# Kernel tuning notes

Hardware: AMD Instinct MI355X
Metric: run time of the kernel (lower is better)

## Reference

```python
import jax, jax.numpy as jnp
import numpy as np
from jax import lax

B, P, ENC, DEC, ATT, EMB, V, L = 64, 196, 2048, 512, 512, 512, 10000, 30


def setup_inputs() -> dict:
    key = jax.random.key(0)
    ks = jax.random.split(key, 24)
    s = 0.02
    encoder_out = jax.random.normal(ks[0], (B, P, ENC), dtype=jnp.float32)
    encoded_captions = jax.random.randint(ks[1], (B, L), 0, V, dtype=jnp.int64)
    caption_lengths = jax.random.randint(ks[2], (B, 1), 2, L + 1, dtype=jnp.int64)
    # ensure max decode length == L-1 (matches torch max(decode_lengths))
    caption_lengths = caption_lengths.at[0, 0].set(L)
    p = lambda k, sh: jax.random.normal(k, sh, dtype=jnp.float32) * s
    return {
        "encoder_out": encoder_out,
        "encoded_captions": encoded_captions,
        "caption_lengths": caption_lengths,
        "W_enc": p(ks[3], (ATT, ENC)), "b_enc": jnp.zeros((ATT,), jnp.float32),
        "W_dec": p(ks[4], (ATT, DEC)), "b_dec": jnp.zeros((ATT,), jnp.float32),
        "w_full": p(ks[5], (ATT,)), "b_full": jnp.zeros((), jnp.float32),
        "emb_table": jax.random.uniform(ks[6], (V, EMB), jnp.float32, -0.1, 0.1),
        "W_ih": p(ks[7], (4 * DEC, EMB + ENC)), "b_ih": jnp.zeros((4 * DEC,), jnp.float32),
        "W_hh": p(ks[8], (4 * DEC, DEC)), "b_hh": jnp.zeros((4 * DEC,), jnp.float32),
        "W_init_h": p(ks[9], (DEC, ENC)), "b_init_h": jnp.zeros((DEC,), jnp.float32),
        "W_init_c": p(ks[10], (DEC, ENC)), "b_init_c": jnp.zeros((DEC,), jnp.float32),
        "W_beta": p(ks[11], (ENC, DEC)), "b_beta": jnp.zeros((ENC,), jnp.float32),
        "W_fc": jax.random.uniform(ks[12], (V, DEC), jnp.float32, -0.1, 0.1),
        "b_fc": jnp.zeros((V,), jnp.float32),
    }


def reference(encoder_out, encoded_captions, caption_lengths,
              W_enc, b_enc, W_dec, b_dec, w_full, b_full, emb_table,
              W_ih, b_ih, W_hh, b_hh, W_init_h, b_init_h, W_init_c, b_init_c,
              W_beta, b_beta, W_fc, b_fc):
    lengths = caption_lengths[:, 0]
    sort_ind = jnp.argsort(-lengths)  # descending, stable
    enc = encoder_out[sort_ind]            # [B,P,ENC]
    caps = encoded_captions[sort_ind]      # [B,L]
    dec_lens = lengths[sort_ind] - 1       # [B]
    T = caps.shape[1] - 1

    embs = emb_table[caps]                 # [B,L,EMB]
    mean_enc = enc.mean(axis=1)
    h0 = mean_enc @ W_init_h.T + b_init_h
    c0 = mean_enc @ W_init_c.T + b_init_c
    # encoder attention projection is h-independent: compute once
    att1 = jnp.einsum('bpe,ae->bpa', enc, W_enc) + b_enc  # [B,P,ATT]

    def step(carry, xs):
        h, c = carry
        emb_t, mask_t = xs  # [B,EMB], [B] bool
        att2 = h @ W_dec.T + b_dec                              # [B,ATT]
        e = jax.nn.relu(att1 + att2[:, None, :]) @ w_full + b_full  # [B,P]
        alpha = jax.nn.softmax(e, axis=1)
        awe = jnp.einsum('bp,bpe->be', alpha, enc)              # [B,ENC]
        gate = jax.nn.sigmoid(h @ W_beta.T + b_beta)
        awe = gate * awe
        x = jnp.concatenate([emb_t, awe], axis=1)               # [B,EMB+ENC]
        gates = x @ W_ih.T + b_ih + h @ W_hh.T + b_hh           # [B,4D]
        i, f, g, o = jnp.split(gates, 4, axis=1)
        i, f, o = jax.nn.sigmoid(i), jax.nn.sigmoid(f), jax.nn.sigmoid(o)
        g = jnp.tanh(g)
        c_new = f * c + i * g
        h_new = o * jnp.tanh(c_new)
        preds = h_new @ W_fc.T + b_fc                           # [B,V]  (dropout: eval/identity)
        m = mask_t[:, None].astype(preds.dtype)
        return (h_new, c_new), (preds * m, alpha * m)

    mask = jnp.arange(T)[:, None] < dec_lens[None, :]           # [T,B]
    embs_t = jnp.swapaxes(embs[:, :T], 0, 1)                    # [T,B,EMB]
    _, (preds, alphas) = lax.scan(step, (h0, c0), (embs_t, mask))
    predictions = jnp.swapaxes(preds, 0, 1)                     # [B,T,V]
    alphas = jnp.swapaxes(alphas, 0, 1)                         # [B,T,P]
    return predictions, alphas, caps, dec_lens, sort_ind
```

## Files before the change

### kernel.cpp

```cpp
#include <hip/hip_runtime.h>
#include <hip/hip_bf16.h>
#include <math.h>
#include <float.h>

#define BDIM   64
#define PDIM   196
#define ENC    2048
#define DECD   512
#define ATTD   512
#define EMBD   512
#define VOC    10000
#define LCAP   30
#define TSTEPS 29

typedef __attribute__((ext_vector_type(8))) short s8v;
typedef __attribute__((ext_vector_type(4))) float f4v;

__device__ __forceinline__ float sigf(float x) { return 1.0f / (1.0f + expf(-x)); }
__device__ __forceinline__ float bf2f(ushort u) { return __uint_as_float(((uint)u) << 16); }

template <int MF, int NIT>
__device__ __forceinline__ void gemm_seg(const __hip_bfloat16* const* arow,
                                         const __hip_bfloat16* const* wrow,
                                         f4v acc[][4]) {
    s8v aP[3][MF], bP[3][4];
    auto LD = [&](int it, int slot) {
#pragma unroll
        for (int mi = 0; mi < MF; ++mi) aP[slot][mi] = *(const s8v*)(arow[mi] + it * 32);
#pragma unroll
        for (int ni = 0; ni < 4; ++ni)  bP[slot][ni] = *(const s8v*)(wrow[ni] + it * 32);
    };
    LD(0, 0);
    if constexpr (NIT > 1) LD(1, 1);
#pragma unroll
    for (int it = 0; it < NIT; ++it) {
        if (it + 2 < NIT) LD(it + 2, (it + 2) % 3);
        const int s = it % 3;
#pragma unroll
        for (int mi = 0; mi < MF; ++mi)
#pragma unroll
            for (int ni = 0; ni < 4; ++ni)
                acc[mi][ni] = __builtin_amdgcn_mfma_f32_16x16x32_bf16(aP[s][mi], bP[s][ni], acc[mi][ni], 0, 0, 0);
    }
}

__global__ void sort_kernel(const int* __restrict__ cap_len,
                            const int* __restrict__ caps,
                            int* __restrict__ sort_ind,
                            int* __restrict__ dec_lens,
                            int* __restrict__ caps_s,
                            float* __restrict__ out_caps,
                            float* __restrict__ out_dlen,
                            float* __restrict__ out_sind) {
    int i = threadIdx.x;
    __shared__ int len[BDIM];
    len[i] = cap_len[i];
    __syncthreads();
    int li = len[i];
    int r = 0;
    for (int j = 0; j < BDIM; ++j) {
        int lj = len[j];
        if (lj > li || (lj == li && j < i)) ++r;
    }
    sort_ind[r] = i;
    dec_lens[r] = li - 1;
    out_sind[r] = (float)i;
    out_dlen[r] = (float)(li - 1);
    for (int tt = 0; tt < LCAP; ++tt) {
        int v = caps[i * LCAP + tt];
        caps_s[r * LCAP + tt] = v;
        out_caps[r * LCAP + tt] = (float)v;
    }
}

__global__ __launch_bounds__(256) void conv_enc_kernel(const float* __restrict__ enc,
                                                       const int* __restrict__ sort_ind,
                                                       __hip_bfloat16* __restrict__ enc_s,
                                                       float* __restrict__ mean_enc) {
    int b = blockIdx.y, tid = threadIdx.x;
    int e = (blockIdx.x << 8) + tid;
    const float* ep = enc + (size_t)sort_ind[b] * (PDIM * ENC) + e;
    __hip_bfloat16* op = enc_s + (size_t)b * (PDIM * ENC) + e;
    float s = 0.f;
    for (int p = 0; p < PDIM; ++p) {
        float v = ep[(size_t)p * ENC];
        s += v;
        op[(size_t)p * ENC] = __float2bfloat16(v);
    }
    mean_enc[(size_t)b * ENC + e] = s * (1.0f / (float)PDIM);
}

__global__ __launch_bounds__(256) void f2b_kernel(const float* __restrict__ src,
                                                  __hip_bfloat16* __restrict__ dst, int n) {
    int i = blockIdx.x * 256 + threadIdx.x;
    if (i < n) dst[i] = __float2bfloat16(src[i]);
}

__global__ __launch_bounds__(256) void h0_kernel(const float* __restrict__ h0f,
                                                 __hip_bfloat16* __restrict__ xh) {
    int idx = blockIdx.x * 256 + threadIdx.x;
    int b = idx >> 9, j = idx & 511;
    xh[(size_t)b * 3072 + 2560 + j] = __float2bfloat16(h0f[idx]);
}

__global__ __launch_bounds__(256) void gemm32_k(
    const float* __restrict__ A, int lda,
    const float* __restrict__ W0, const float* __restrict__ bias0,
    float* __restrict__ C, int ldc, int K) {
    __shared__ float As[16][64];
    __shared__ float Ws[16][64];
    const int tid = threadIdx.x;
    const int tx = tid & 15, ty = tid >> 4;
    const int bn0 = blockIdx.x * 64;
    const int lr = tid >> 2;
    const int lk = (tid & 3) << 2;
    const float* Arow = A + (size_t)lr * lda;
    const int wn = bn0 + lr;
    float acc[4][4];
#pragma unroll
    for (int i = 0; i < 4; ++i)
#pragma unroll
        for (int j = 0; j < 4; ++j) acc[i][j] = 0.f;
    for (int k0 = 0; k0 < K; k0 += 16) {
        float4 av = *(const float4*)(Arow + k0 + lk);
        float4 wv = *(const float4*)(W0 + (size_t)wn * K + k0 + lk);
        __syncthreads();
        As[lk + 0][lr] = av.x; As[lk + 1][lr] = av.y;
        As[lk + 2][lr] = av.z; As[lk + 3][lr] = av.w;
        Ws[lk + 0][lr] = wv.x; Ws[lk + 1][lr] = wv.y;
        Ws[lk + 2][lr] = wv.z; Ws[lk + 3][lr] = wv.w;
        __syncthreads();
#pragma unroll
        for (int kk = 0; kk < 16; ++kk) {
            const float4 a = *(const float4*)&As[kk][ty << 2];
            const float4 w = *(const float4*)&Ws[kk][tx << 2];
            acc[0][0] += a.x * w.x; acc[0][1] += a.x * w.y; acc[0][2] += a.x * w.z; acc[0][3] += a.x * w.w;
            acc[1][0] += a.y * w.x; acc[1][1] += a.y * w.y; acc[1][2] += a.y * w.z; acc[1][3] += a.y * w.w;
            acc[2][0] += a.z * w.x; acc[2][1] += a.z * w.y; acc[2][2] += a.z * w.z; acc[2][3] += a.z * w.w;
            acc[3][0] += a.w * w.x; acc[3][1] += a.w * w.y; acc[3][2] += a.w * w.z; acc[3][3] += a.w * w.w;
        }
    }
#pragma unroll
    for (int i = 0; i < 4; ++i) {
        int row = (ty << 2) + i;
#pragma unroll
        for (int j = 0; j < 4; ++j) {
            int col = bn0 + (tx << 2) + j;
            C[(size_t)row * ldc + col] = acc[i][j] + bias0[col];
        }
    }
}

__global__ __launch_bounds__(64) void att1_gemm(
    const __hip_bfloat16* __restrict__ A, const __hip_bfloat16* __restrict__ W,
    const float* __restrict__ bias, __hip_bfloat16* __restrict__ C) {
    const int l = threadIdx.x, c16 = l & 15, kg = l >> 4;
    const int m0 = blockIdx.x * 32, n0 = blockIdx.y * 64;
    f4v acc[2][4];
#pragma unroll
    for (int mi = 0; mi < 2; ++mi)
#pragma unroll
        for (int ni = 0; ni < 4; ++ni) acc[mi][ni] = (f4v)0.0f;
    const __hip_bfloat16* arow[2];
#pragma unroll
    for (int mi = 0; mi < 2; ++mi)
        arow[mi] = A + (size_t)(m0 + mi * 16 + c16) * ENC + kg * 8;
    const __hip_bfloat16* wrow[4];
#pragma unroll
    for (int ni = 0; ni < 4; ++ni)
        wrow[ni] = W + (size_t)(n0 + ni * 16 + c16) * ENC + kg * 8;
    gemm_seg<2, 64>(arow, wrow, acc);
#pragma unroll
    for (int mi = 0; mi < 2; ++mi)
#pragma unroll
        for (int ni = 0; ni < 4; ++ni)
#pragma unroll
            for (int i = 0; i < 4; ++i) {
                int r = m0 + mi * 16 + kg * 4 + i;
                int c = n0 + ni * 16 + c16;
                C[(size_t)r * 512 + c] = __float2bfloat16(acc[mi][ni][i] + bias[c]);
            }
}

__global__ __launch_bounds__(64) void gact_gemm(
    const __hip_bfloat16* __restrict__ H,
    const __hip_bfloat16* __restrict__ Wb,
    const __hip_bfloat16* __restrict__ Wd,
    float* __restrict__ P) {
    const int l = threadIdx.x, c16 = l & 15, kg = l >> 4;
    const int n0 = blockIdx.x * 64, m0 = blockIdx.y * 16, z = blockIdx.z;
    const int ko = z * 256;
    f4v acc[1][4];
#pragma unroll
    for (int ni = 0; ni < 4; ++ni) acc[0][ni] = (f4v)0.0f;
    const __hip_bfloat16* arow[1] = { H + (size_t)(m0 + c16) * 3072 + ko + kg * 8 };
    const __hip_bfloat16* wrow[4];
#pragma unroll
    for (int ni = 0; ni < 4; ++ni) {
        int n = n0 + ni * 16 + c16;
        wrow[ni] = ((n < 2048) ? Wb + (size_t)n * 512 : Wd + (size_t)(n - 2048) * 512) + ko + kg * 8;
    }
    gemm_seg<1, 8>(arow, wrow, acc);
    float* Pz = P + (size_t)z * (64 * 2560);
#pragma unroll
    for (int ni = 0; ni < 4; ++ni)
#pragma unroll
        for (int i = 0; i < 4; ++i) {
            int r = m0 + kg * 4 + i;
            int c = n0 + ni * 16 + c16;
            Pz[(size_t)r * 2560 + c] = acc[0][ni][i];
        }
}

__global__ __launch_bounds__(64) void gates_gemm(
    const __hip_bfloat16* __restrict__ X,
    const __hip_bfloat16* __restrict__ Wih,
    const __hip_bfloat16* __restrict__ Whh,
    float* __restrict__ P) {
    const int l = threadIdx.x, c16 = l & 15, kg = l >> 4;
    const int n0 = blockIdx.x * 64, m0 = blockIdx.y * 16, z = blockIdx.z;
    f4v acc[1][4];
#pragma unroll
    for (int ni = 0; ni < 4; ++ni) acc[0][ni] = (f4v)0.0f;
    const __hip_bfloat16* arow[1];
    const __hip_bfloat16* wrow[4];
    if (z == 0) {
        arow[0] = X + (size_t)(m0 + c16) * 3072 + kg * 8;
#pragma unroll
        for (int ni = 0; ni < 4; ++ni)
            wrow[ni] = Wih + (size_t)(n0 + ni * 16 + c16) * 2560 + kg * 8;
        gemm_seg<1, 48>(arow, wrow, acc);
    } else {
        arow[0] = X + (size_t)(m0 + c16) * 3072 + 1536 + kg * 8;
#pragma unroll
        for (int ni = 0; ni < 4; ++ni)
            wrow[ni] = Wih + (size_t)(n0 + ni * 16 + c16) * 2560 + 1536 + kg * 8;
        gemm_seg<1, 32>(arow, wrow, acc);
        arow[0] = X + (size_t)(m0 + c16) * 3072 + 2560 + kg * 8;
#pragma unroll
        for (int ni = 0; ni < 4; ++ni)
            wrow[ni] = Whh + (size_t)(n0 + ni * 16 + c16) * 512 + kg * 8;
        gemm_seg<1, 16>(arow, wrow, acc);
    }
    float* Pz = P + (size_t)z * (64 * 2048);
#pragma unroll
    for (int ni = 0; ni < 4; ++ni)
#pragma unroll
        for (int i = 0; i < 4; ++i) {
            int r = m0 + kg * 4 + i;
            int c = n0 + ni * 16 + c16;
            Pz[(size_t)r * 2048 + c] = acc[0][ni][i];
        }
}

__global__ __launch_bounds__(64) void predsb_gemm(
    const __hip_bfloat16* __restrict__ Hs,
    const __hip_bfloat16* __restrict__ Wfc,
    const float* __restrict__ bias,
    const int* __restrict__ dec_lens,
    float* __restrict__ out) {
    const int l = threadIdx.x, c16 = l & 15, kg = l >> 4;
    const int n0 = blockIdx.x * 64, m0 = blockIdx.y * 32;
    f4v acc[2][4];
#pragma unroll
    for (int mi = 0; mi < 2; ++mi)
#pragma unroll
        for (int ni = 0; ni < 4; ++ni) acc[mi][ni] = (f4v)0.0f;
    const __hip_bfloat16* arow[2];
#pragma unroll
    for (int mi = 0; mi < 2; ++mi)
        arow[mi] = Hs + (size_t)(m0 + mi * 16 + c16) * 512 + kg * 8;
    const __hip_bfloat16* wrow[4];
#pragma unroll
    for (int ni = 0; ni < 4; ++ni) {
        int n = n0 + ni * 16 + c16;
        int nn = (n < VOC) ? n : (VOC - 1);
        wrow[ni] = Wfc + (size_t)nn * 512 + kg * 8;
    }
    gemm_seg<2, 16>(arow, wrow, acc);
#pragma unroll
    for (int mi = 0; mi < 2; ++mi)
#pragma unroll
        for (int ni = 0; ni < 4; ++ni)
#pragma unroll
            for (int i = 0; i < 4; ++i) {
                int r = m0 + mi * 16 + kg * 4 + i;
                int c = n0 + ni * 16 + c16;
                if (c < VOC) {
                    int tt = r >> 6, b = r & 63;
                    float v = acc[mi][ni][i] + bias[c];
                    out[(size_t)b * (TSTEPS * VOC) + (size_t)tt * VOC + c] =
                        (tt < dec_lens[b]) ? v : 0.f;
                }
            }
}

__global__ __launch_bounds__(256) void attawe_kernel(
    const __hip_bfloat16* __restrict__ att1, const float* __restrict__ gactp,
    const __hip_bfloat16* __restrict__ enc_s,
    const float* __restrict__ w_full, const float* __restrict__ b_full,
    const float* __restrict__ b_dec, const float* __restrict__ b_beta,
    const float* __restrict__ emb_table,
    const int* __restrict__ caps_s, const int* __restrict__ dec_lens,
    __hip_bfloat16* __restrict__ xh, float* __restrict__ out_alphas, int t) {
    const int G = 64 * 2560;
    int b = blockIdx.x;
    int tid = threadIdx.x;
    __shared__ float s_att2[ATTD];
    __shared__ float s_wf[ATTD];
    __shared__ float s_e[PDIM];
    __shared__ float red[256];

    const float* gb = gactp + (size_t)b * 2560;
    s_att2[tid]       = gb[2048 + tid]       + gb[G + 2048 + tid]       + b_dec[tid];
    s_att2[tid + 256] = gb[2048 + 256 + tid] + gb[G + 2048 + 256 + tid] + b_dec[256 + tid];
    s_wf[tid]       = w_full[tid];
    s_wf[tid + 256] = w_full[tid + 256];
    __syncthreads();

    int wv = tid >> 6, lane = tid & 63;
    const float bf = b_full[0];
    const int a0 = lane << 3;
    for (int p = wv; p < PDIM; p += 4) {
        const ushort* row = (const ushort*)att1 + ((size_t)b * PDIM + p) * ATTD + a0;
        float s = 0.f;
#pragma unroll
        for (int i = 0; i < 8; ++i) {
            float x = bf2f(row[i]) + s_att2[a0 + i];
            s += fmaxf(x, 0.f) * s_wf[a0 + i];
        }
#pragma unroll
        for (int off = 32; off; off >>= 1) s += __shfl_xor(s, off);
        if (lane == 0) s_e[p] = s + bf;
    }
    __syncthreads();

    float v = (tid < PDIM) ? s_e[tid] : -FLT_MAX;
    red[tid] = v;
    __syncthreads();
    for (int st = 128; st; st >>= 1) {
        if (tid < st) red[tid] = fmaxf(red[tid], red[tid + st]);
        __syncthreads();
    }
    float mx = red[0];
    __syncthreads();
    float ex = (tid < PDIM) ? expf(v - mx) : 0.f;
    red[tid] = ex;
    __syncthreads();
    for (int st = 128; st; st >>= 1) {
        if (tid < st) red[tid] += red[tid + st];
        __syncthreads();
    }
    float inv = 1.f / red[0];
    __syncthreads();
    if (tid < PDIM) {
        float al = ex * inv;
        s_e[tid] = al;
        out_alphas[(size_t)b * (TSTEPS * PDIM) + (size_t)t * PDIM + tid] =
            (t < dec_lens[b]) ? al : 0.f;
    }
    __syncthreads();

    int e = tid << 3;
    const ushort* ep = (const ushort*)enc_s + (size_t)b * (PDIM * ENC) + e;
    float acc[8];
#pragma unroll
    for (int i = 0; i < 8; ++i) acc[i] = 0.f;
#pragma unroll 2
    for (int p = 0; p < PDIM; ++p) {
        float al = s_e[p];
        s8v u = *(const s8v*)(ep + (size_t)p * ENC);
#pragma unroll
        for (int i = 0; i < 8; ++i) acc[i] += al * bf2f((ushort)u[i]);
    }
    float4 p00 = *(const float4*)(gb + e);
    float4 p01 = *(const float4*)(gb + e + 4);
    float4 p10 = *(const float4*)(gb + G + e);
    float4 p11 = *(const float4*)(gb + G + e + 4);
    float4 bb0 = *(const float4*)(b_beta + e);
    float4 bb1 = *(const float4*)(b_beta + e + 4);
    float g[8];
    g[0] = sigf(p00.x + p10.x + bb0.x); g[1] = sigf(p00.y + p10.y + bb0.y);
    g[2] = sigf(p00.z + p10.z + bb0.z); g[3] = sigf(p00.w + p10.w + bb0.w);
    g[4] = sigf(p01.x + p11.x + bb1.x); g[5] = sigf(p01.y + p11.y + bb1.y);
    g[6] = sigf(p01.z + p11.z + bb1.z); g[7] = sigf(p01.w + p11.w + bb1.w);
    __hip_bfloat16 ob[8];
#pragma unroll
    for (int i = 0; i < 8; ++i) ob[i] = __float2bfloat16(acc[i] * g[i]);
    *(uint4*)(xh + (size_t)b * 3072 + 512 + e) = *(uint4*)ob;

    if (tid < 128) {
        int cap = caps_s[b * LCAP + t];
        int j = tid << 2;
        float4 em = *(const float4*)(emb_table + (size_t)cap * EMBD + j);
        __hip_bfloat16 eb[4];
        eb[0] = __float2bfloat16(em.x); eb[1] = __float2bfloat16(em.y);
        eb[2] = __float2bfloat16(em.z); eb[3] = __float2bfloat16(em.w);
        *(uint2*)(xh + (size_t)b * 3072 + j) = *(uint2*)eb;
    }
}

__global__ __launch_bounds__(256) void cell_kernel(
    const float* __restrict__ gatesp, const float* __restrict__ b_ih,
    const float* __restrict__ b_hh, float* __restrict__ c,
    __hip_bfloat16* __restrict__ xh, __hip_bfloat16* __restrict__ hstore, int t) {
    const int GS = 64 * 2048;
    int idx = blockIdx.x * 256 + threadIdx.x;
    int b = idx >> 9, j = idx & 511;
    const float* g0 = gatesp + (size_t)b * 2048;
    const float* g1 = gatesp + GS + (size_t)b * 2048;
    float vi = g0[j]        + g1[j]        + b_ih[j]        + b_hh[j];
    float vf = g0[512 + j]  + g1[512 + j]  + b_ih[512 + j]  + b_hh[512 + j];
    float vg = g0[1024 + j] + g1[1024 + j] + b_ih[1024 + j] + b_hh[1024 + j];
    float vo = g0[1536 + j] + g1[1536 + j] + b_ih[1536 + j] + b_hh[1536 + j];
    float i_ = sigf(vi), f_ = sigf(vf), gg = tanhf(vg), o_ = sigf(vo);
    float cn = f_ * c[idx] + i_ * gg;
    c[idx] = cn;
    __hip_bfloat16 hb = __float2bfloat16(o_ * tanhf(cn));
    xh[(size_t)b * 3072 + 2560 + j] = hb;
    hstore[(size_t)t * (64 * 512) + idx] = hb;
}

extern "C" void kernel_launch(void* const* d_in, const int* in_sizes, int n_in,
                              void* d_out, int out_size, void* d_ws, size_t ws_size,
                              hipStream_t stream) {
    const float* enc      = (const float*)d_in[0];
    const int*   caps     = (const int*)d_in[1];
    const int*   clen     = (const int*)d_in[2];
    const float* W_enc    = (const float*)d_in[3];
    const float* b_enc    = (const float*)d_in[4];
    const float* W_dec    = (const float*)d_in[5];
    const float* b_dec    = (const float*)d_in[6];
    const float* w_full   = (const float*)d_in[7];
    const float* b_full   = (const float*)d_in[8];
    const float* emb_tab  = (const float*)d_in[9];
    const float* W_ih     = (const float*)d_in[10];
    const float* b_ih     = (const float*)d_in[11];
    const float* W_hh     = (const float*)d_in[12];
    const float* b_hh     = (const float*)d_in[13];
    const float* W_init_h = (const float*)d_in[14];
    const float* b_init_h = (const float*)d_in[15];
    const float* W_init_c = (const float*)d_in[16];
    const float* b_init_c = (const float*)d_in[17];
    const float* W_beta   = (const float*)d_in[18];
    const float* b_beta   = (const float*)d_in[19];
    const float* W_fc     = (const float*)d_in[20];
    const float* b_fc     = (const float*)d_in[21];

    float* out_pred = (float*)d_out;
    float* out_alph = out_pred + (size_t)BDIM * TSTEPS * VOC;
    float* out_caps = out_alph + (size_t)BDIM * TSTEPS * PDIM;
    float* out_dlen = out_caps + BDIM * LCAP;
    float* out_sind = out_dlen + BDIM;

    char* p = (char*)d_ws;
    auto carve = [&](size_t bytes) { char* r = p; p += (bytes + 255) & ~(size_t)255; return r; };
    int* sort_ind = (int*)carve(64 * 4);
    int* dec_lens = (int*)carve(64 * 4);
    int* caps_s   = (int*)carve(64 * LCAP * 4);
    float* mean_e = (float*)carve((size_t)64 * ENC * 4);
    float* h0f    = (float*)carve((size_t)64 * 512 * 4);
    float* cbuf   = (float*)carve((size_t)64 * 512 * 4);
    float* gactp  = (float*)carve((size_t)2 * 64 * 2560 * 4);
    float* gatesp = (float*)carve((size_t)2 * 64 * 2048 * 4);
    __hip_bfloat16* xh     = (__hip_bfloat16*)carve((size_t)64 * 3072 * 2);
    __hip_bfloat16* hstore = (__hip_bfloat16*)carve((size_t)TSTEPS * 64 * 512 * 2);
    __hip_bfloat16* enc_s  = (__hip_bfloat16*)carve((size_t)64 * PDIM * ENC * 2);
    __hip_bfloat16* att1   = (__hip_bfloat16*)carve((size_t)64 * PDIM * 512 * 2);
    __hip_bfloat16* Wb_enc = (__hip_bfloat16*)carve((size_t)512 * 2048 * 2);
    __hip_bfloat16* Wb_bet = (__hip_bfloat16*)carve((size_t)2048 * 512 * 2);
    __hip_bfloat16* Wb_dec = (__hip_bfloat16*)carve((size_t)512 * 512 * 2);
    __hip_bfloat16* Wb_ih  = (__hip_bfloat16*)carve((size_t)2048 * 2560 * 2);
    __hip_bfloat16* Wb_hh  = (__hip_bfloat16*)carve((size_t)2048 * 512 * 2);
    __hip_bfloat16* Wb_fc  = (__hip_bfloat16*)carve((size_t)VOC * 512 * 2);

    sort_kernel<<<1, 64, 0, stream>>>(clen, caps, sort_ind, dec_lens, caps_s,
                                      out_caps, out_dlen, out_sind);
    conv_enc_kernel<<<dim3(8, 64), 256, 0, stream>>>(enc, sort_ind, enc_s, mean_e);
    f2b_kernel<<<(512 * 2048 + 255) / 256, 256, 0, stream>>>(W_enc, Wb_enc, 512 * 2048);
    f2b_kernel<<<(2048 * 512 + 255) / 256, 256, 0, stream>>>(W_beta, Wb_bet, 2048 * 512);
    f2b_kernel<<<(512 * 512 + 255) / 256, 256, 0, stream>>>(W_dec, Wb_dec, 512 * 512);
    f2b_kernel<<<(2048 * 2560 + 255) / 256, 256, 0, stream>>>(W_ih, Wb_ih, 2048 * 2560);
    f2b_kernel<<<(2048 * 512 + 255) / 256, 256, 0, stream>>>(W_hh, Wb_hh, 2048 * 512);
    f2b_kernel<<<(VOC * 512 + 255) / 256, 256, 0, stream>>>(W_fc, Wb_fc, VOC * 512);

    gemm32_k<<<dim3(8, 1), 256, 0, stream>>>(mean_e, ENC, W_init_h, b_init_h, h0f, 512, ENC);
    gemm32_k<<<dim3(8, 1), 256, 0, stream>>>(mean_e, ENC, W_init_c, b_init_c, cbuf, 512, ENC);
    h0_kernel<<<128, 256, 0, stream>>>(h0f, xh);

    att1_gemm<<<dim3(392, 8), 64, 0, stream>>>(enc_s, Wb_enc, b_enc, att1);

    for (int t = 0; t < TSTEPS; ++t) {
        gact_gemm<<<dim3(40, 4, 2), 64, 0, stream>>>(xh + 2560, Wb_bet, Wb_dec, gactp);
        attawe_kernel<<<64, 256, 0, stream>>>(att1, gactp, enc_s, w_full, b_full,
                                              b_dec, b_beta, emb_tab, caps_s,
                                              dec_lens, xh, out_alph, t);
        gates_gemm<<<dim3(32, 4, 2), 64, 0, stream>>>(xh, Wb_ih, Wb_hh, gatesp);
        cell_kernel<<<128, 256, 0, stream>>>(gatesp, b_ih, b_hh, cbuf, xh, hstore, t);
    }

    predsb_gemm<<<dim3(160, 58), 64, 0, stream>>>(hstore, Wb_fc, b_fc, dec_lens, out_pred);
}
```

Baseline: 3.251 ms.

## Fuse per-step decode kernels into one persistent cooperative kernel with grid syncs

Replaces the four launches per time step with a single cooperative persistent kernel of 256 blocks. Each step runs three phases separated by grid.sync: an h-projection GEMM fused across W_beta, W_dec and W_hh, attention plus gated awe split four ways per batch row, and the W_ih GEMM with the LSTM cell fused in. Embeddings are gathered once up front, split-K partial buffers are removed, and att1_gemm uses larger M tiles. The aim is to cut launch overhead and intermediate traffic, at the cost of grid-wide barriers and low occupancy in phases 1 and 3; a non-cooperative fallback path is kept.

After: 7.351 ms. +126.1%, slower.

```diff
diff --git a/kernel.cpp b/kernel.cpp
--- a/kernel.cpp
+++ b/kernel.cpp
@@ -1,7 +1,10 @@
 #include <hip/hip_runtime.h>
 #include <hip/hip_bf16.h>
+#include <hip/hip_cooperative_groups.h>
 #include <math.h>
 #include <float.h>
+
+namespace cg = cooperative_groups;
 
 #define BDIM   64
 #define PDIM   196
@@ -19,16 +22,16 @@
 __device__ __forceinline__ float sigf(float x) { return 1.0f / (1.0f + expf(-x)); }
 __device__ __forceinline__ float bf2f(ushort u) { return __uint_as_float(((uint)u) << 16); }
 
-template <int MF, int NIT>
+template <int MF, int NF, int NIT>
 __device__ __forceinline__ void gemm_seg(const __hip_bfloat16* const* arow,
                                          const __hip_bfloat16* const* wrow,
-                                         f4v acc[][4]) {
-    s8v aP[3][MF], bP[3][4];
+                                         f4v acc[][NF]) {
+    s8v aP[3][MF], bP[3][NF];
     auto LD = [&](int it, int slot) {
 #pragma unroll
         for (int mi = 0; mi < MF; ++mi) aP[slot][mi] = *(const s8v*)(arow[mi] + it * 32);
 #pragma unroll
-        for (int ni = 0; ni < 4; ++ni)  bP[slot][ni] = *(const s8v*)(wrow[ni] + it * 32);
+        for (int ni = 0; ni < NF; ++ni) bP[slot][ni] = *(const s8v*)(wrow[ni] + it * 32);
     };
     LD(0, 0);
     if constexpr (NIT > 1) LD(1, 1);
@@ -39,9 +42,224 @@
 #pragma unroll
         for (int mi = 0; mi < MF; ++mi)
 #pragma unroll
-            for (int ni = 0; ni < 4; ++ni)
+            for (int ni = 0; ni < NF; ++ni)
                 acc[mi][ni] = __builtin_amdgcn_mfma_f32_16x16x32_bf16(aP[s][mi], bP[s][ni], acc[mi][ni], 0, 0, 0);
     }
+}
+
+
+__device__ __forceinline__ void phase1(int bid, int tid,
+    const __hip_bfloat16* hbuf, const __hip_bfloat16* Wb_bet,
+    const __hip_bfloat16* Wb_dec, const __hip_bfloat16* Wb_hh, float* C_h) {
+    const int l = tid & 63, c16 = l & 15, kg = l >> 4, w = tid >> 6;
+    const int n0 = bid * 64;
+    f4v acc[1][4];
+#pragma unroll
+    for (int ni = 0; ni < 4; ++ni) acc[0][ni] = (f4v)0.0f;
+    const __hip_bfloat16* arow[1] = { hbuf + (size_t)(w * 16 + c16) * 512 + kg * 8 };
+    const __hip_bfloat16* wrow[4];
+#pragma unroll
+    for (int ni = 0; ni < 4; ++ni) {
+        int n = n0 + ni * 16 + c16;
+        const __hip_bfloat16* wr;
+        if (n < 2048)      wr = Wb_bet + (size_t)n * 512;
+        else if (n < 2560) wr = Wb_dec + (size_t)(n - 2048) * 512;
+        else               wr = Wb_hh + (size_t)(n - 2560) * 512;
+        wrow[ni] = wr + kg * 8;
+    }
+    gemm_seg<1, 4, 16>(arow, wrow, acc);
+#pragma unroll
+    for (int ni = 0; ni < 4; ++ni)
+#pragma unroll
+        for (int i = 0; i < 4; ++i)
+            C_h[(size_t)(w * 16 + kg * 4 + i) * 4608 + n0 + ni * 16 + c16] = acc[0][ni][i];
+}
+
+__device__ __forceinline__ void phase2(int bid, int tid, float* smem,
+    const __hip_bfloat16* att1, const __hip_bfloat16* enc_s, const float* C_h,
+    const float* w_full, const float* b_full, const float* b_dec,
+    const float* b_beta, const int* dec_lens,
+    __hip_bfloat16* awebuf, float* out_alphas, int t) {
+    const int b = bid >> 2, q = bid & 3;
+    const int l = tid & 63, w = tid >> 6;
+    float* s_att2 = smem;
+    float* s_wf   = smem + 512;
+    float* s_e    = smem + 1024;
+    float* red    = smem + 1280;
+    float* s_part = smem + 1536;
+
+    s_att2[tid]       = C_h[(size_t)b * 4608 + 2048 + tid]       + b_dec[tid];
+    s_att2[tid + 256] = C_h[(size_t)b * 4608 + 2048 + 256 + tid] + b_dec[256 + tid];
+    s_wf[tid]       = w_full[tid];
+    s_wf[tid + 256] = w_full[tid + 256];
+    __syncthreads();
+
+    const float bf = b_full[0];
+    const int a0 = l << 3;
+    for (int p = w; p < PDIM; p += 4) {
+        const ushort* row = (const ushort*)att1 + ((size_t)b * PDIM + p) * 512 + a0;
+        s8v u = *(const s8v*)row;
+        float s = 0.f;
+#pragma unroll
+        for (int i = 0; i < 8; ++i) {
+            float x = bf2f((ushort)u[i]) + s_att2[a0 + i];
+            s += fmaxf(x, 0.f) * s_wf[a0 + i];
+        }
+#pragma unroll
+        for (int off = 32; off; off >>= 1) s += __shfl_xor(s, off);
+        if (l == 0) s_e[p] = s + bf;
+    }
+    __syncthreads();
+
+    float v = (tid < PDIM) ? s_e[tid] : -FLT_MAX;
+    red[tid] = v;
+    __syncthreads();
+    for (int st = 128; st; st >>= 1) {
+        if (tid < st) red[tid] = fmaxf(red[tid], red[tid + st]);
+        __syncthreads();
+    }
+    float mx = red[0];
+    __syncthreads();
+    float ex = (tid < PDIM) ? expf(v - mx) : 0.f;
+    red[tid] = ex;
+    __syncthreads();
+    for (int st = 128; st; st >>= 1) {
+        if (tid < st) red[tid] += red[tid + st];
+        __syncthreads();
+    }
+    float inv = 1.f / red[0];
+    __syncthreads();
+    if (tid < PDIM) {
+        float al = ex * inv;
+        s_e[tid] = al;
+        if (q == 0)
+            out_alphas[(size_t)b * (TSTEPS * PDIM) + (size_t)t * PDIM + tid] =
+                (t < dec_lens[b]) ? al : 0.f;
+    }
+    __syncthreads();
+
+    const int c0 = q * 512 + l * 8;
+    const ushort* ep = (const ushort*)enc_s + (size_t)b * (PDIM * ENC) + c0;
+    float a8[8];
+#pragma unroll
+    for (int i = 0; i < 8; ++i) a8[i] = 0.f;
+    for (int p = w * 49; p < w * 49 + 49; ++p) {
+        float al = s_e[p];
+        s8v u = *(const s8v*)(ep + (size_t)p * ENC);
+#pragma unroll
+        for (int i = 0; i < 8; ++i) a8[i] += al * bf2f((ushort)u[i]);
+    }
+#pragma unroll
+    for (int i = 0; i < 8; ++i) s_part[w * 512 + l * 8 + i] = a8[i];
+    __syncthreads();
+#pragma unroll
+    for (int u2 = 0; u2 < 2; ++u2) {
+        int cc = tid * 2 + u2;
+        float s = s_part[cc] + s_part[512 + cc] + s_part[1024 + cc] + s_part[1536 + cc];
+        int gcol = q * 512 + cc;
+        float gate = sigf(C_h[(size_t)b * 4608 + gcol] + b_beta[gcol]);
+        awebuf[(size_t)b * 2048 + gcol] = __float2bfloat16(s * gate);
+    }
+}
+
+__device__ __forceinline__ void phase3(int bid, int tid, float* smem,
+    const __hip_bfloat16* awebuf, const __hip_bfloat16* embs_all,
+    const __hip_bfloat16* Wb_ih, const float* C_h,
+    const float* b_ih, const float* b_hh,
+    float* cbuf, __hip_bfloat16* hbuf, __hip_bfloat16* hstore, int t) {
+    const int l = tid & 63, c16 = l & 15, kg = l >> 4, w = tid >> 6;
+    const int j0 = bid * 16;
+    f4v acc[4][1];
+#pragma unroll
+    for (int mi = 0; mi < 4; ++mi) acc[mi][0] = (f4v)0.0f;
+    const __hip_bfloat16* arow[4];
+    const __hip_bfloat16* wrow[1];
+    const __hip_bfloat16* wbase = Wb_ih + (size_t)(512 * w + j0 + c16) * 2560;
+#pragma unroll
+    for (int mi = 0; mi < 4; ++mi)
+        arow[mi] = embs_all + ((size_t)t * 64 + mi * 16 + c16) * 512 + kg * 8;
+    wrow[0] = wbase + kg * 8;
+    gemm_seg<4, 1, 16>(arow, wrow, acc);
+#pragma unroll
+    for (int mi = 0; mi < 4; ++mi)
+        arow[mi] = awebuf + (size_t)(mi * 16 + c16) * 2048 + kg * 8;
+    wrow[0] = wbase + 512 + kg * 8;
+    gemm_seg<4, 1, 64>(arow, wrow, acc);
+#pragma unroll
+    for (int mi = 0; mi < 4; ++mi)
+#pragma unroll
+        for (int i = 0; i < 4; ++i)
+            smem[w * 1024 + (mi * 16 + kg * 4 + i) * 16 + c16] = acc[mi][0][i];
+    __syncthreads();
+#pragma unroll
+    for (int u2 = 0; u2 < 4; ++u2) {
+        int pid = u2 * 256 + tid;
+        int b = pid >> 4, jj = pid & 15;
+        float vg[4];
+#pragma unroll
+        for (int g = 0; g < 4; ++g) {
+            int col = 512 * g + j0 + jj;
+            vg[g] = smem[g * 1024 + b * 16 + jj]
+                  + C_h[(size_t)b * 4608 + 2560 + col]
+                  + b_ih[col] + b_hh[col];
+        }
+        float i_ = sigf(vg[0]), f_ = sigf(vg[1]), gg = tanhf(vg[2]), o_ = sigf(vg[3]);
+        int cidx = b * 512 + j0 + jj;
+        float cn = f_ * cbuf[cidx] + i_ * gg;
+        cbuf[cidx] = cn;
+        __hip_bfloat16 hb = __float2bfloat16(o_ * tanhf(cn));
+        hbuf[cidx] = hb;
+        hstore[(size_t)t * (64 * 512) + cidx] = hb;
+    }
+}
+
+__global__ __launch_bounds__(256) void decode_kernel(
+    const __hip_bfloat16* att1, const __hip_bfloat16* enc_s,
+    const __hip_bfloat16* embs_all, const __hip_bfloat16* Wb_bet,
+    const __hip_bfloat16* Wb_dec, const __hip_bfloat16* Wb_hh,
+    const __hip_bfloat16* Wb_ih, const float* b_dec, const float* b_beta,
+    const float* b_full, const float* w_full, const float* b_ih,
+    const float* b_hh, const int* dec_lens, __hip_bfloat16* hbuf,
+    float* cbuf, float* C_h, __hip_bfloat16* awebuf,
+    __hip_bfloat16* hstore, float* out_alphas) {
+    cg::grid_group grid = cg::this_grid();
+    __shared__ float smem[4096];
+    const int tid = threadIdx.x, bid = blockIdx.x;
+#pragma unroll 1
+    for (int t = 0; t < TSTEPS; ++t) {
+        if (bid < 72) phase1(bid, tid, hbuf, Wb_bet, Wb_dec, Wb_hh, C_h);
+        grid.sync();
+        phase2(bid, tid, smem, att1, enc_s, C_h, w_full, b_full, b_dec, b_beta,
+               dec_lens, awebuf, out_alphas, t);
+        grid.sync();
+        if (bid < 32) phase3(bid, tid, smem, awebuf, embs_all, Wb_ih, C_h,
+                             b_ih, b_hh, cbuf, hbuf, hstore, t);
+        grid.sync();
+    }
+}
+
+__global__ __launch_bounds__(256) void p1_kernel(
+    const __hip_bfloat16* hbuf, const __hip_bfloat16* Wb_bet,
+    const __hip_bfloat16* Wb_dec, const __hip_bfloat16* Wb_hh, float* C_h) {
+    phase1(blockIdx.x, threadIdx.x, hbuf, Wb_bet, Wb_dec, Wb_hh, C_h);
+}
+__global__ __launch_bounds__(256) void p2_kernel(
+    const __hip_bfloat16* att1, const __hip_bfloat16* enc_s, const float* C_h,
+    const float* w_full, const float* b_full, const float* b_dec,
+    const float* b_beta, const int* dec_lens,
+    __hip_bfloat16* awebuf, float* out_alphas, int t) {
+    __shared__ float smem[4096];
+    phase2(blockIdx.x, threadIdx.x, smem, att1, enc_s, C_h, w_full, b_full,
+           b_dec, b_beta, dec_lens, awebuf, out_alphas, t);
+}
+__global__ __launch_bounds__(256) void p3_kernel(
+    const __hip_bfloat16* awebuf, const __hip_bfloat16* embs_all,
+    const __hip_bfloat16* Wb_ih, const float* C_h,
+    const float* b_ih, const float* b_hh,
+    float* cbuf, __hip_bfloat16* hbuf, __hip_bfloat16* hstore, int t) {
+    __shared__ float smem[4096];
+    phase3(blockIdx.x, threadIdx.x, smem, awebuf, embs_all, Wb_ih, C_h,
+           b_ih, b_hh, cbuf, hbuf, hstore, t);
 }
 
 __global__ void sort_kernel(const int* __restrict__ cap_len,
@@ -96,11 +314,22 @@
     if (i < n) dst[i] = __float2bfloat16(src[i]);
 }
 
-__global__ __launch_bounds__(256) void h0_kernel(const float* __restrict__ h0f,
-                                                 __hip_bfloat16* __restrict__ xh) {
+__global__ __launch_bounds__(256) void h0b_kernel(const float* __restrict__ h0f,
+                                                  __hip_bfloat16* __restrict__ hbuf) {
     int idx = blockIdx.x * 256 + threadIdx.x;
-    int b = idx >> 9, j = idx & 511;
-    xh[(size_t)b * 3072 + 2560 + j] = __float2bfloat16(h0f[idx]);
+    hbuf[idx] = __float2bfloat16(h0f[idx]);
+}
+
+__global__ __launch_bounds__(256) void embgather_kernel(
+    const float* __restrict__ emb_table, const int* __restrict__ caps_s,
+    __hip_bfloat16* __restrict__ embs_all) {
+    int b = blockIdx.x, t = blockIdx.y;
+    int cap = caps_s[b * LCAP + t];
+    int j = threadIdx.x << 1;
+    float2 e = *(const float2*)(emb_table + (size_t)cap * EMBD + j);
+    __hip_bfloat16 eb[2];
+    eb[0] = __float2bfloat16(e.x); eb[1] = __float2bfloat16(e.y);
+    *(uint*)(embs_all + ((size_t)t * 64 + b) * 512 + j) = *(uint*)eb;
 }
 
 __global__ __launch_bounds__(256) void gemm32_k(
@@ -155,23 +384,23 @@
     const __hip_bfloat16* __restrict__ A, const __hip_bfloat16* __restrict__ W,
     const float* __restrict__ bias, __hip_bfloat16* __restrict__ C) {
     const int l = threadIdx.x, c16 = l & 15, kg = l >> 4;
-    const int m0 = blockIdx.x * 32, n0 = blockIdx.y * 64;
-    f4v acc[2][4];
-#pragma unroll
-    for (int mi = 0; mi < 2; ++mi)
+    const int m0 = blockIdx.x * 64, n0 = blockIdx.y * 64;
+    f4v acc[4][4];
+#pragma unroll
+    for (int mi = 0; mi < 4; ++mi)
 #pragma unroll
         for (int ni = 0; ni < 4; ++ni) acc[mi][ni] = (f4v)0.0f;
-    const __hip_bfloat16* arow[2];
-#pragma unroll
-    for (int mi = 0; mi < 2; ++mi)
+    const __hip_bfloat16* arow[4];
+#pragma unroll
+    for (int mi = 0; mi < 4; ++mi)
         arow[mi] = A + (size_t)(m0 + mi * 16 + c16) * ENC + kg * 8;
     const __hip_bfloat16* wrow[4];
 #pragma unroll
     for (int ni = 0; ni < 4; ++ni)
         wrow[ni] = W + (size_t)(n0 + ni * 16 + c16) * ENC + kg * 8;
-    gemm_seg<2, 64>(arow, wrow, acc);
-#pragma unroll
-    for (int mi = 0; mi < 2; ++mi)
+    gemm_seg<4, 4, 64>(arow, wrow, acc);
+#pragma unroll
+    for (int mi = 0; mi < 4; ++mi)
 #pragma unroll
         for (int ni = 0; ni < 4; ++ni)
 #pragma unroll
@@ -180,77 +409,6 @@
                 int c = n0 + ni * 16 + c16;
                 C[(size_t)r * 512 + c] = __float2bfloat16(acc[mi][ni][i] + bias[c]);
             }
-}
-
-__global__ __launch_bounds__(64) void gact_gemm(
-    const __hip_bfloat16* __restrict__ H,
-    const __hip_bfloat16* __restrict__ Wb,
-    const __hip_bfloat16* __restrict__ Wd,
-    float* __restrict__ P) {
-    const int l = threadIdx.x, c16 = l & 15, kg = l >> 4;
-    const int n0 = blockIdx.x * 64, m0 = blockIdx.y * 16, z = blockIdx.z;
-    const int ko = z * 256;
-    f4v acc[1][4];
-#pragma unroll
-    for (int ni = 0; ni < 4; ++ni) acc[0][ni] = (f4v)0.0f;
-    const __hip_bfloat16* arow[1] = { H + (size_t)(m0 + c16) * 3072 + ko + kg * 8 };
-    const __hip_bfloat16* wrow[4];
-#pragma unroll
-    for (int ni = 0; ni < 4; ++ni) {
-        int n = n0 + ni * 16 + c16;
-        wrow[ni] = ((n < 2048) ? Wb + (size_t)n * 512 : Wd + (size_t)(n - 2048) * 512) + ko + kg * 8;
-    }
-    gemm_seg<1, 8>(arow, wrow, acc);
-    float* Pz = P + (size_t)z * (64 * 2560);
-#pragma unroll
-    for (int ni = 0; ni < 4; ++ni)
-#pragma unroll
-        for (int i = 0; i < 4; ++i) {
-            int r = m0 + kg * 4 + i;
-            int c = n0 + ni * 16 + c16;
-            Pz[(size_t)r * 2560 + c] = acc[0][ni][i];
-        }
-}
-
-__global__ __launch_bounds__(64) void gates_gemm(
-    const __hip_bfloat16* __restrict__ X,
-    const __hip_bfloat16* __restrict__ Wih,
-    const __hip_bfloat16* __restrict__ Whh,
-    float* __restrict__ P) {
-    const int l = threadIdx.x, c16 = l & 15, kg = l >> 4;
-    const int n0 = blockIdx.x * 64, m0 = blockIdx.y * 16, z = blockIdx.z;
-    f4v acc[1][4];
-#pragma unroll
-    for (int ni = 0; ni < 4; ++ni) acc[0][ni] = (f4v)0.0f;
-    const __hip_bfloat16* arow[1];
-    const __hip_bfloat16* wrow[4];
-    if (z == 0) {
-        arow[0] = X + (size_t)(m0 + c16) * 3072 + kg * 8;
-#pragma unroll
-        for (int ni = 0; ni < 4; ++ni)
-            wrow[ni] = Wih + (size_t)(n0 + ni * 16 + c16) * 2560 + kg * 8;
-        gemm_seg<1, 48>(arow, wrow, acc);
-    } else {
-        arow[0] = X + (size_t)(m0 + c16) * 3072 + 1536 + kg * 8;
-#pragma unroll
-        for (int ni = 0; ni < 4; ++ni)
-            wrow[ni] = Wih + (size_t)(n0 + ni * 16 + c16) * 2560 + 1536 + kg * 8;
-        gemm_seg<1, 32>(arow, wrow, acc);
-        arow[0] = X + (size_t)(m0 + c16) * 3072 + 2560 + kg * 8;
-#pragma unroll
-        for (int ni = 0; ni < 4; ++ni)
-            wrow[ni] = Whh + (size_t)(n0 + ni * 16 + c16) * 512 + kg * 8;
-        gemm_seg<1, 16>(arow, wrow, acc);
-    }
-    float* Pz = P + (size_t)z * (64 * 2048);
-#pragma unroll
-    for (int ni = 0; ni < 4; ++ni)
-#pragma unroll
-        for (int i = 0; i < 4; ++i) {
-            int r = m0 + kg * 4 + i;
-            int c = n0 + ni * 16 + c16;
-            Pz[(size_t)r * 2048 + c] = acc[0][ni][i];
-        }
 }
 
 __global__ __launch_bounds__(64) void predsb_gemm(
@@ -277,7 +435,7 @@
         int nn = (n < VOC) ? n : (VOC - 1);
         wrow[ni] = Wfc + (size_t)nn * 512 + kg * 8;
     }
-    gemm_seg<2, 16>(arow, wrow, acc);
+    gemm_seg<2, 4, 16>(arow, wrow, acc);
 #pragma unroll
     for (int mi = 0; mi < 2; ++mi)
 #pragma unroll
@@ -293,132 +451,6 @@
                         (tt < dec_lens[b]) ? v : 0.f;
                 }
             }
-}
-
-__global__ __launch_bounds__(256) void attawe_kernel(
-    const __hip_bfloat16* __restrict__ att1, const float* __restrict__ gactp,
-    const __hip_bfloat16* __restrict__ enc_s,
-    const float* __restrict__ w_full, const float* __restrict__ b_full,
-    const float* __restrict__ b_dec, const float* __restrict__ b_beta,
-    const float* __restrict__ emb_table,
-    const int* __restrict__ caps_s, const int* __restrict__ dec_lens,
-    __hip_bfloat16* __restrict__ xh, float* __restrict__ out_alphas, int t) {
-    const int G = 64 * 2560;
-    int b = blockIdx.x;
-    int tid = threadIdx.x;
-    __shared__ float s_att2[ATTD];
-    __shared__ float s_wf[ATTD];
-    __shared__ float s_e[PDIM];
-    __shared__ float red[256];
-
-    const float* gb = gactp + (size_t)b * 2560;
-    s_att2[tid]       = gb[2048 + tid]       + gb[G + 2048 + tid]       + b_dec[tid];
-    s_att2[tid + 256] = gb[2048 + 256 + tid] + gb[G + 2048 + 256 + tid] + b_dec[256 + tid];
-    s_wf[tid]       = w_full[tid];
-    s_wf[tid + 256] = w_full[tid + 256];
-    __syncthreads();
-
-    int wv = tid >> 6, lane = tid & 63;
-    const float bf = b_full[0];
-    const int a0 = lane << 3;
-    for (int p = wv; p < PDIM; p += 4) {
-        const ushort* row = (const ushort*)att1 + ((size_t)b * PDIM + p) * ATTD + a0;
-        float s = 0.f;
-#pragma unroll
-        for (int i = 0; i < 8; ++i) {
-            float x = bf2f(row[i]) + s_att2[a0 + i];
-            s += fmaxf(x, 0.f) * s_wf[a0 + i];
-        }
-#pragma unroll
-        for (int off = 32; off; off >>= 1) s += __shfl_xor(s, off);
-        if (lane == 0) s_e[p] = s + bf;
-    }
-    __syncthreads();
-
-    float v = (tid < PDIM) ? s_e[tid] : -FLT_MAX;
-    red[tid] = v;
-    __syncthreads();
-    for (int st = 128; st; st >>= 1) {
-        if (tid < st) red[tid] = fmaxf(red[tid], red[tid + st]);
-        __syncthreads();
-    }
-    float mx = red[0];
-    __syncthreads();
-    float ex = (tid < PDIM) ? expf(v - mx) : 0.f;
-    red[tid] = ex;
-    __syncthreads();
-    for (int st = 128; st; st >>= 1) {
-        if (tid < st) red[tid] += red[tid + st];
-        __syncthreads();
-    }
-    float inv = 1.f / red[0];
-    __syncthreads();
-    if (tid < PDIM) {
-        float al = ex * inv;
-        s_e[tid] = al;
-        out_alphas[(size_t)b * (TSTEPS * PDIM) + (size_t)t * PDIM + tid] =
-            (t < dec_lens[b]) ? al : 0.f;
-    }
-    __syncthreads();
-
-    int e = tid << 3;
-    const ushort* ep = (const ushort*)enc_s + (size_t)b * (PDIM * ENC) + e;
-    float acc[8];
-#pragma unroll
-    for (int i = 0; i < 8; ++i) acc[i] = 0.f;
-#pragma unroll 2
-    for (int p = 0; p < PDIM; ++p) {
-        float al = s_e[p];
-        s8v u = *(const s8v*)(ep + (size_t)p * ENC);
-#pragma unroll
-        for (int i = 0; i < 8; ++i) acc[i] += al * bf2f((ushort)u[i]);
-    }
-    float4 p00 = *(const float4*)(gb + e);
-    float4 p01 = *(const float4*)(gb + e + 4);
-    float4 p10 = *(const float4*)(gb + G + e);
-    float4 p11 = *(const float4*)(gb + G + e + 4);
-    float4 bb0 = *(const float4*)(b_beta + e);
-    float4 bb1 = *(const float4*)(b_beta + e + 4);
-    float g[8];
-    g[0] = sigf(p00.x + p10.x + bb0.x); g[1] = sigf(p00.y + p10.y + bb0.y);
-    g[2] = sigf(p00.z + p10.z + bb0.z); g[3] = sigf(p00.w + p10.w + bb0.w);
-    g[4] = sigf(p01.x + p11.x + bb1.x); g[5] = sigf(p01.y + p11.y + bb1.y);
-    g[6] = sigf(p01.z + p11.z + bb1.z); g[7] = sigf(p01.w + p11.w + bb1.w);
-    __hip_bfloat16 ob[8];
-#pragma unroll
-    for (int i = 0; i < 8; ++i) ob[i] = __float2bfloat16(acc[i] * g[i]);
-    *(uint4*)(xh + (size_t)b * 3072 + 512 + e) = *(uint4*)ob;
-
-    if (tid < 128) {
-        int cap = caps_s[b * LCAP + t];
-        int j = tid << 2;
-        float4 em = *(const float4*)(emb_table + (size_t)cap * EMBD + j);
-        __hip_bfloat16 eb[4];
-        eb[0] = __float2bfloat16(em.x); eb[1] = __float2bfloat16(em.y);
-        eb[2] = __float2bfloat16(em.z); eb[3] = __float2bfloat16(em.w);
-        *(uint2*)(xh + (size_t)b * 3072 + j) = *(uint2*)eb;
-    }
-}
-
-__global__ __launch_bounds__(256) void cell_kernel(
-    const float* __restrict__ gatesp, const float* __restrict__ b_ih,
-    const float* __restrict__ b_hh, float* __restrict__ c,
-    __hip_bfloat16* __restrict__ xh, __hip_bfloat16* __restrict__ hstore, int t) {
-    const int GS = 64 * 2048;
-    int idx = blockIdx.x * 256 + threadIdx.x;
-    int b = idx >> 9, j = idx & 511;
-    const float* g0 = gatesp + (size_t)b * 2048;
-    const float* g1 = gatesp + GS + (size_t)b * 2048;
-    float vi = g0[j]        + g1[j]        + b_ih[j]        + b_hh[j];
-    float vf = g0[512 + j]  + g1[512 + j]  + b_ih[512 + j]  + b_hh[512 + j];
-    float vg = g0[1024 + j] + g1[1024 + j] + b_ih[1024 + j] + b_hh[1024 + j];
-    float vo = g0[1536 + j] + g1[1536 + j] + b_ih[1536 + j] + b_hh[1536 + j];
-    float i_ = sigf(vi), f_ = sigf(vf), gg = tanhf(vg), o_ = sigf(vo);
-    float cn = f_ * c[idx] + i_ * gg;
-    c[idx] = cn;
-    __hip_bfloat16 hb = __float2bfloat16(o_ * tanhf(cn));
-    xh[(size_t)b * 3072 + 2560 + j] = hb;
-    hstore[(size_t)t * (64 * 512) + idx] = hb;
 }
 
 extern "C" void kernel_launch(void* const* d_in, const int* in_sizes, int n_in,
@@ -458,12 +490,12 @@
     int* sort_ind = (int*)carve(64 * 4);
     int* dec_lens = (int*)carve(64 * 4);
     int* caps_s   = (int*)carve(64 * LCAP * 4);
+    float* cbuf   = (float*)carve((size_t)64 * 512 * 4);
+    float* C_h    = (float*)carve((size_t)64 * 4608 * 4);
     float* mean_e = (float*)carve((size_t)64 * ENC * 4);
     float* h0f    = (float*)carve((size_t)64 * 512 * 4);
-    float* cbuf   = (float*)carve((size_t)64 * 512 * 4);
-    float* gactp  = (float*)carve((size_t)2 * 64 * 2560 * 4);
-    float* gatesp = (float*)carve((size_t)2 * 64 * 2048 * 4);
-    __hip_bfloat16* xh     = (__hip_bfloat16*)carve((size_t)64 * 3072 * 2);
+    __hip_bfloat16* hbuf   = (__hip_bfloat16*)carve((size_t)64 * 512 * 2);
+    __hip_bfloat16* awebuf = (__hip_bfloat16*)carve((size_t)64 * 2048 * 2);
     __hip_bfloat16* hstore = (__hip_bfloat16*)carve((size_t)TSTEPS * 64 * 512 * 2);
     __hip_bfloat16* enc_s  = (__hip_bfloat16*)carve((size_t)64 * PDIM * ENC * 2);
     __hip_bfloat16* att1   = (__hip_bfloat16*)carve((size_t)64 * PDIM * 512 * 2);
@@ -473,6 +505,7 @@
     __hip_bfloat16* Wb_ih  = (__hip_bfloat16*)carve((size_t)2048 * 2560 * 2);
     __hip_bfloat16* Wb_hh  = (__hip_bfloat16*)carve((size_t)2048 * 512 * 2);
     __hip_bfloat16* Wb_fc  = (__hip_bfloat16*)carve((size_t)VOC * 512 * 2);
+    __hip_bfloat16* embs_all = Wb_enc;
 
     sort_kernel<<<1, 64, 0, stream>>>(clen, caps, sort_ind, dec_lens, caps_s,
                                       out_caps, out_dlen, out_sind);
@@ -486,17 +519,31 @@
 
     gemm32_k<<<dim3(8, 1), 256, 0, stream>>>(mean_e, ENC, W_init_h, b_init_h, h0f, 512, ENC);
     gemm32_k<<<dim3(8, 1), 256, 0, stream>>>(mean_e, ENC, W_init_c, b_init_c, cbuf, 512, ENC);
-    h0_kernel<<<128, 256, 0, stream>>>(h0f, xh);
-
-    att1_gemm<<<dim3(392, 8), 64, 0, stream>>>(enc_s, Wb_enc, b_enc, att1);
-
-    for (int t = 0; t < TSTEPS; ++t) {
-        gact_gemm<<<dim3(40, 4, 2), 64, 0, stream>>>(xh + 2560, Wb_bet, Wb_dec, gactp);
-        attawe_kernel<<<64, 256, 0, stream>>>(att1, gactp, enc_s, w_full, b_full,
-                                              b_dec, b_beta, emb_tab, caps_s,
-                                              dec_lens, xh, out_alph, t);
-        gates_gemm<<<dim3(32, 4, 2), 64, 0, stream>>>(xh, Wb_ih, Wb_hh, gatesp);
-        cell_kernel<<<128, 256, 0, stream>>>(gatesp, b_ih, b_hh, cbuf, xh, hstore, t);
+    h0b_kernel<<<128, 256, 0, stream>>>(h0f, hbuf);
+
+    att1_gemm<<<dim3(196, 8), 64, 0, stream>>>(enc_s, Wb_enc, b_enc, att1);
+
+    embgather_kernel<<<dim3(64, TSTEPS), 256, 0, stream>>>(emb_tab, caps_s, embs_all);
+
+    void* kargs[] = {
+        (void*)&att1, (void*)&enc_s, (void*)&embs_all,
+        (void*)&Wb_bet, (void*)&Wb_dec, (void*)&Wb_hh, (void*)&Wb_ih,
+        (void*)&b_dec, (void*)&b_beta, (void*)&b_full, (void*)&w_full,
+        (void*)&b_ih, (void*)&b_hh, (void*)&dec_lens,
+        (void*)&hbuf, (void*)&cbuf, (void*)&C_h, (void*)&awebuf,
+        (void*)&hstore, (void*)&out_alph };
+    hipError_t cerr = hipLaunchCooperativeKernel((void*)decode_kernel, dim3(256),
+                                                 dim3(256), kargs, 0, stream);
+    if (cerr != hipSuccess) {
+        (void)hipGetLastError();
+        for (int t = 0; t < TSTEPS; ++t) {
+            p1_kernel<<<72, 256, 0, stream>>>(hbuf, Wb_bet, Wb_dec, Wb_hh, C_h);
+            p2_kernel<<<256, 256, 0, stream>>>(att1, enc_s, C_h, w_full, b_full,
+                                               b_dec, b_beta, dec_lens, awebuf,
+                                               out_alph, t);
+            p3_kernel<<<32, 256, 0, stream>>>(awebuf, embs_all, Wb_ih, C_h,
+                                              b_ih, b_hh, cbuf, hbuf, hstore, t);
+        }
     }
 
     predsb_gemm<<<dim3(160, 58), 64, 0, stream>>>(hstore, Wb_fc, b_fc, dec_lens, out_pred);
```
